# Optimization experiments

Measured on AMD Instinct MI355X. Metric: run time of the kernel, lower is better.

## Reference

```python
import jax, jax.numpy as jnp
import numpy as np
import math

DIM = 1024
NUM_HEADS = 16
HEAD_DIM = DIM // NUM_HEADS
BLOCK_SIZE = 64


def _block_mask(src_blocks, tgt_blocks, num_blocks):
    # Block-level BigBird mask: global first/last block columns, sliding window of 1, random blocks.
    i = jnp.arange(num_blocks)[:, None]
    j = jnp.arange(num_blocks)[None, :]
    band = jnp.abs(i - j) <= 1
    glob = (j == 0) | (j == num_blocks - 1)
    bm = band | glob
    bm = bm.at[src_blocks, tgt_blocks].set(True)
    return bm  # [nb, nb] bool


def setup_inputs() -> dict:
    key = jax.random.key(0)
    ks = jax.random.split(key, 12)
    B, S = 2, 2048
    x = jax.random.normal(ks[0], (B, S, DIM), dtype=jnp.float32)
    scale = 0.02
    Wq = jax.random.normal(ks[1], (DIM, DIM), dtype=jnp.float32) * scale
    bq = jnp.zeros((DIM,), dtype=jnp.float32)
    Wk = jax.random.normal(ks[2], (DIM, DIM), dtype=jnp.float32) * scale
    bk = jnp.zeros((DIM,), dtype=jnp.float32)
    Wv = jax.random.normal(ks[3], (DIM, DIM), dtype=jnp.float32) * scale
    bv = jnp.zeros((DIM,), dtype=jnp.float32)
    Wo = jax.random.normal(ks[4], (DIM, DIM), dtype=jnp.float32) * scale
    bo = jnp.zeros((DIM,), dtype=jnp.float32)
    num_blocks = S // BLOCK_SIZE
    src_blocks = jax.random.randint(ks[5], (3,), 0, num_blocks, dtype=jnp.int32)
    tgt_blocks = jax.random.randint(ks[6], (3,), 0, num_blocks, dtype=jnp.int32)
    return {"x": x, "Wq": Wq, "bq": bq, "Wk": Wk, "bk": bk, "Wv": Wv, "bv": bv,
            "Wo": Wo, "bo": bo, "src_blocks": src_blocks, "tgt_blocks": tgt_blocks}


def reference(x, Wq, bq, Wk, bk, Wv, bv, Wo, bo, src_blocks, tgt_blocks):
    B, S, _ = x.shape
    nb = S // BLOCK_SIZE
    # NOTE: original torch code uses .view (not transpose) to split heads; replicate faithfully.
    q = (x @ Wq.T + bq).reshape(B, NUM_HEADS, S, HEAD_DIM)
    k = (x @ Wk.T + bk).reshape(B, NUM_HEADS, S, HEAD_DIM)
    v = (x @ Wv.T + bv).reshape(B, NUM_HEADS, S, HEAD_DIM)
    bm = _block_mask(src_blocks, tgt_blocks, nb)
    mask = jnp.repeat(jnp.repeat(bm, BLOCK_SIZE, axis=0), BLOCK_SIZE, axis=1)  # [S, S]
    scores = jnp.einsum('bhqd,bhkd->bhqk', q, k) / math.sqrt(HEAD_DIM)
    scores = jnp.where(mask[None, None], scores, jnp.float32(-1e9))
    attn = jax.nn.softmax(scores, axis=-1)
    out = jnp.einsum('bhqk,bhkd->bhqd', attn, v)
    out = out.transpose(0, 2, 1, 3).reshape(B, S, DIM)
    return out @ Wo.T + bo
```

## Files before the change

kernel.cpp:

```cpp
#include <hip/hip_runtime.h>
#include <math.h>

typedef __attribute__((ext_vector_type(8))) short short8;
typedef __attribute__((ext_vector_type(4))) float f32x4;

#define SEQ 2048
#define NB  32

__device__ __forceinline__ unsigned short f2bf(float f) {
    unsigned u = __float_as_uint(f);
    u = (u + 0x7FFFu + ((u >> 16) & 1u)) >> 16;
    return (unsigned short)u;
}

__device__ __forceinline__ void gload16(const unsigned short* g, unsigned short* l) {
    __builtin_amdgcn_global_load_lds(
        (__attribute__((address_space(1))) void*)(void*)(g),
        (__attribute__((address_space(3))) void*)(l), 16, 0, 0);
}

__global__ __launch_bounds__(256) void cvt_bf16(const float* __restrict__ in,
                                                unsigned short* __restrict__ out, int n8) {
    int i = blockIdx.x * 256 + threadIdx.x;
    const int stride = gridDim.x * 256;
    for (; i < n8; i += stride) {
        const float4 a = ((const float4*)in)[i * 2];
        const float4 b = ((const float4*)in)[i * 2 + 1];
        uint4 o;
        o.x = f2bf(a.x) | ((unsigned)f2bf(a.y) << 16);
        o.y = f2bf(a.z) | ((unsigned)f2bf(a.w) << 16);
        o.z = f2bf(b.x) | ((unsigned)f2bf(b.y) << 16);
        o.w = f2bf(b.z) | ((unsigned)f2bf(b.w) << 16);
        ((uint4*)out)[i] = o;
    }
}

__global__ __launch_bounds__(256) void cvt_w4(const float* __restrict__ w0,
                                              const float* __restrict__ w1,
                                              const float* __restrict__ w2,
                                              const float* __restrict__ w3,
                                              unsigned short* __restrict__ o0,
                                              unsigned short* __restrict__ o1,
                                              unsigned short* __restrict__ o2,
                                              unsigned short* __restrict__ o3) {
    const int which = blockIdx.y;
    const float* in = (which == 0) ? w0 : (which == 1) ? w1 : (which == 2) ? w2 : w3;
    unsigned short* out = (which == 0) ? o0 : (which == 1) ? o1 : (which == 2) ? o2 : o3;
    int i = blockIdx.x * 256 + threadIdx.x;
    const int stride = gridDim.x * 256;
    for (; i < 131072; i += stride) {
        const float4 a = ((const float4*)in)[i * 2];
        const float4 b = ((const float4*)in)[i * 2 + 1];
        uint4 o;
        o.x = f2bf(a.x) | ((unsigned)f2bf(a.y) << 16);
        o.y = f2bf(a.z) | ((unsigned)f2bf(a.w) << 16);
        o.z = f2bf(b.x) | ((unsigned)f2bf(b.y) << 16);
        o.w = f2bf(b.z) | ((unsigned)f2bf(b.w) << 16);
        ((uint4*)out)[i] = o;
    }
}

template <int BF16OUT, int BN>
__global__ __launch_bounds__(256) void gemm_bt(const unsigned short* __restrict__ A,
                                               const unsigned short* __restrict__ Wall,
                                               const float* __restrict__ b0,
                                               const float* __restrict__ b1,
                                               const float* __restrict__ b2,
                                               unsigned short* __restrict__ outb,
                                               float* __restrict__ outf) {
    constexpr int MI = (BN == 128) ? 4 : 2;
    constexpr int NI = 4;
    __shared__ __align__(16) unsigned short As[2][128 * 32];
    __shared__ __align__(16) unsigned short Bs[2][BN * 32];

    const int t = threadIdx.x;
    const int w = t >> 6, l = t & 63;
    const int bx = blockIdx.x;
    const int which = (BN == 128) ? (bx >> 3) : 0;
    const int n0 = (BN == 128) ? (bx & 7) * 128 : bx * 64;
    const int m0 = blockIdx.y * 128;
    const unsigned short* W = Wall + (size_t)which * (1024ull * 1024);
    const float* bias = (which == 0) ? b0 : (which == 1) ? b1 : b2;

    const int wr = (BN == 128) ? (w >> 1) * 64 : w * 32;
    const int wc = (BN == 128) ? (w & 1) * 64 : 0;

    f32x4 acc[MI][NI];
#pragma unroll
    for (int i = 0; i < MI; ++i)
#pragma unroll
        for (int j = 0; j < NI; ++j) acc[i][j] = f32x4{0.f, 0.f, 0.f, 0.f};

    const unsigned short* Ag = A + (size_t)(m0 + w * 32 + (l >> 2)) * 1024 + (l & 3) * 8;
    const unsigned short* Wg =
        W + (size_t)(n0 + ((BN == 128) ? w * 32 : w * 16) + (l >> 2)) * 1024 + (l & 3) * 8;

    auto STAGE = [&](unsigned short* Asb, unsigned short* Bsb, int k0) {
        gload16(Ag + k0, Asb + w * 1024);
        gload16(Ag + k0 + 16 * 1024, Asb + w * 1024 + 512);
        gload16(Wg + k0, Bsb + ((BN == 128) ? w * 1024 : w * 512));
        if (BN == 128) gload16(Wg + k0 + 16 * 1024, Bsb + w * 1024 + 512);
    };
    auto COMPUTE = [&](const unsigned short* Asb, const unsigned short* Bsb) {
        short8 af[MI], bfr[NI];
#pragma unroll
        for (int mi = 0; mi < MI; ++mi)
            af[mi] = *(const short8*)&Asb[(wr + mi * 16 + (l & 15)) * 32 + (l >> 4) * 8];
#pragma unroll
        for (int ni = 0; ni < NI; ++ni)
            bfr[ni] = *(const short8*)&Bsb[(wc + ni * 16 + (l & 15)) * 32 + (l >> 4) * 8];
#pragma unroll
        for (int mi = 0; mi < MI; ++mi)
#pragma unroll
            for (int ni = 0; ni < NI; ++ni)
                acc[mi][ni] = __builtin_amdgcn_mfma_f32_16x16x32_bf16(af[mi], bfr[ni],
                                                                      acc[mi][ni], 0, 0, 0);
    };
#define WAITV_INFLIGHT()                                                  \
    do {                                                                  \
        if constexpr (BN == 128)                                          \
            asm volatile("s_waitcnt vmcnt(4)" ::: "memory");              \
        else                                                              \
            asm volatile("s_waitcnt vmcnt(3)" ::: "memory");              \
        __builtin_amdgcn_sched_barrier(0);                                \
    } while (0)
#define BAR()                                                             \
    do {                                                                  \
        __builtin_amdgcn_s_barrier();                                     \
        __builtin_amdgcn_sched_barrier(0);                                \
    } while (0)
#define READS_DONE_BAR()                                                  \
    do {                                                                  \
        asm volatile("s_waitcnt lgkmcnt(0)" ::: "memory");                \
        __builtin_amdgcn_sched_barrier(0);                                \
        __builtin_amdgcn_s_barrier();                                     \
        __builtin_amdgcn_sched_barrier(0);                                \
    } while (0)

    STAGE(As[0], Bs[0], 0);
#pragma unroll 1
    for (int kt2 = 0; kt2 < 16; ++kt2) {
        STAGE(As[1], Bs[1], (kt2 * 2 + 1) * 32);
        WAITV_INFLIGHT();
        BAR();
        COMPUTE(As[0], Bs[0]);
        READS_DONE_BAR();

        if (kt2 < 15) {
            STAGE(As[0], Bs[0], (kt2 * 2 + 2) * 32);
            WAITV_INFLIGHT();
        } else {
            asm volatile("s_waitcnt vmcnt(0)" ::: "memory");
            __builtin_amdgcn_sched_barrier(0);
        }
        BAR();
        COMPUTE(As[1], Bs[1]);
        if (kt2 < 15) READS_DONE_BAR();
    }
#undef WAITV_INFLIGHT
#undef BAR
#undef READS_DONE_BAR

    const int g = l >> 4, c = l & 15;
#pragma unroll
    for (int ni = 0; ni < NI; ++ni) {
        const int n = n0 + wc + ni * 16 + c;
        const float bv = bias[n];
#pragma unroll
        for (int mi = 0; mi < MI; ++mi) {
#pragma unroll
            for (int j = 0; j < 4; ++j) {
                const size_t m = (size_t)(m0 + wr + mi * 16 + g * 4 + j);
                const float v = acc[mi][ni][j] + bv;
                if (BF16OUT)
                    (outb + (size_t)which * (4096ull * 1024))[m * 1024 + n] = f2bf(v);
                else
                    outf[m * 1024 + n] = v;
            }
        }
    }
}

__global__ __launch_bounds__(256) void transpose_v(const unsigned short* __restrict__ v,
                                                   unsigned short* __restrict__ vt) {
    __shared__ __align__(16) unsigned short L[64][72];
    const int t = threadIdx.x;
    const int st = blockIdx.x;
    const int ht = blockIdx.y;
    const int b = blockIdx.z;
    {
        const int r = t >> 2, cs = t & 3;
        const unsigned short* src =
            v + (size_t)(b * 16 + ht) * (SEQ * 64) + (size_t)(st * 64 + r) * 64 + cs * 16;
        *(uint4*)&L[r][cs * 16] = *(const uint4*)src;
        *(uint4*)&L[r][cs * 16 + 8] = *(const uint4*)(src + 8);
    }
    __syncthreads();
    {
        const int dr = t >> 2, ss = t & 3;
        unsigned short tmp[16];
#pragma unroll
        for (int e = 0; e < 16; ++e) tmp[e] = L[ss * 16 + e][dr];
        unsigned short* dst =
            vt + (size_t)(b * 16 + ht) * (SEQ * 64) + (size_t)dr * SEQ + st * 64 + ss * 16;
        *(uint4*)dst = *(uint4*)&tmp[0];
        *(uint4*)(dst + 8) = *(uint4*)&tmp[8];
    }
}

__global__ __launch_bounds__(256) void attn_mfma(const unsigned short* __restrict__ qb_,
                                                 const unsigned short* __restrict__ kb_,
                                                 const unsigned short* __restrict__ vtb_,
                                                 const int* __restrict__ srcb,
                                                 const int* __restrict__ tgtb,
                                                 unsigned short* __restrict__ outb) {
    __shared__ __align__(16) unsigned short Ks[64 * 72];
    __shared__ __align__(16) unsigned short Vs[64 * 72];
    __shared__ __align__(16) unsigned short Ps[4][16 * 72];

    const int t = threadIdx.x, w = t >> 6, l = t & 63;
    const int qi = blockIdx.x, h = blockIdx.y, b = blockIdx.z;
    const int g = l >> 4, c = l & 15;

    unsigned mask = 1u | (1u << (NB - 1)) | (1u << qi);
    if (qi > 0) mask |= 1u << (qi - 1);
    if (qi < NB - 1) mask |= 1u << (qi + 1);
#pragma unroll
    for (int tt = 0; tt < 3; ++tt)
        if (srcb[tt] == qi) mask |= 1u << (tgtb[tt] & 31);

    const size_t ho = (size_t)(b * 16 + h) * (SEQ * 64);
    const unsigned short* Q = qb_ + ho;
    const unsigned short* K = kb_ + ho;
    const unsigned short* VT = vtb_ + ho;

    short8 qf[2];
    {
        const unsigned short* qrow = Q + (size_t)(qi * 64 + w * 16 + c) * 64;
        qf[0] = *(const short8*)(qrow + g * 8);
        qf[1] = *(const short8*)(qrow + 32 + g * 8);
    }

    f32x4 oacc[4];
#pragma unroll
    for (int d = 0; d < 4; ++d) oacc[d] = f32x4{0.f, 0.f, 0.f, 0.f};
    float mrun = -INFINITY, lsum = 0.f;

    const int sr = t >> 2, sc = (t & 3) * 16;

    for (int kb = 0; kb < NB; ++kb) {
        if (!((mask >> kb) & 1u)) continue;

        const unsigned short* ksrc = K + (size_t)(kb * 64 + sr) * 64 + sc;
        const unsigned short* vsrc = VT + (size_t)sr * SEQ + kb * 64 + sc;
        uint4 k0 = *(const uint4*)ksrc, k1 = *(const uint4*)(ksrc + 8);
        uint4 v0 = *(const uint4*)vsrc, v1 = *(const uint4*)(vsrc + 8);

        __syncthreads();
        *(uint4*)&Ks[sr * 72 + sc] = k0;
        *(uint4*)&Ks[sr * 72 + sc + 8] = k1;
        *(uint4*)&Vs[sr * 72 + sc] = v0;
        *(uint4*)&Vs[sr * 72 + sc + 8] = v1;
        __syncthreads();

        f32x4 sacc[4];
#pragma unroll
        for (int kt = 0; kt < 4; ++kt) sacc[kt] = f32x4{0.f, 0.f, 0.f, 0.f};
#pragma unroll
        for (int kt = 0; kt < 4; ++kt) {
#pragma unroll
            for (int ks = 0; ks < 2; ++ks) {
                const short8 ka = *(const short8*)&Ks[(kt * 16 + c) * 72 + ks * 32 + g * 8];
                sacc[kt] = __builtin_amdgcn_mfma_f32_16x16x32_bf16(ka, qf[ks], sacc[kt], 0, 0, 0);
            }
        }

        float sv[16];
        float tmax = -INFINITY;
#pragma unroll
        for (int kt = 0; kt < 4; ++kt)
#pragma unroll
            for (int j = 0; j < 4; ++j) {
                const float x = sacc[kt][j] * 0.125f;
                sv[kt * 4 + j] = x;
                tmax = fmaxf(tmax, x);
            }
        tmax = fmaxf(tmax, __shfl_xor(tmax, 16));
        tmax = fmaxf(tmax, __shfl_xor(tmax, 32));
        const float newm = fmaxf(mrun, tmax);
        const float corr = __expf(mrun - newm);
        float ps = 0.f;
#pragma unroll
        for (int e = 0; e < 16; ++e) {
            const float p = __expf(sv[e] - newm);
            sv[e] = p;
            ps += p;
        }
        ps += __shfl_xor(ps, 16);
        ps += __shfl_xor(ps, 32);
        lsum = lsum * corr + ps;
        mrun = newm;
#pragma unroll
        for (int d = 0; d < 4; ++d)
#pragma unroll
            for (int j = 0; j < 4; ++j) oacc[d][j] *= corr;

        unsigned short* pw = &Ps[w][c * 72];
#pragma unroll
        for (int kt = 0; kt < 4; ++kt) {
            uint2 pk;
            pk.x = f2bf(sv[kt * 4 + 0]) | ((unsigned)f2bf(sv[kt * 4 + 1]) << 16);
            pk.y = f2bf(sv[kt * 4 + 2]) | ((unsigned)f2bf(sv[kt * 4 + 3]) << 16);
            *(uint2*)&pw[kt * 16 + g * 4] = pk;
        }
        asm volatile("s_waitcnt lgkmcnt(0)" ::: "memory");
        __builtin_amdgcn_sched_barrier(0);

#pragma unroll
        for (int ks = 0; ks < 2; ++ks) {
            const short8 pb = *(const short8*)&Ps[w][c * 72 + ks * 32 + g * 8];
#pragma unroll
            for (int dt = 0; dt < 4; ++dt) {
                const short8 va = *(const short8*)&Vs[(dt * 16 + c) * 72 + ks * 32 + g * 8];
                oacc[dt] = __builtin_amdgcn_mfma_f32_16x16x32_bf16(va, pb, oacc[dt], 0, 0, 0);
            }
        }
    }

    const float inv = 1.f / lsum;
    unsigned short* orow = outb + (size_t)(b * SEQ + qi * 64 + w * 16 + c) * 1024 + h * 64;
#pragma unroll
    for (int dt = 0; dt < 4; ++dt)
#pragma unroll
        for (int j = 0; j < 4; ++j)
            orow[dt * 16 + g * 4 + j] = f2bf(oacc[dt][j] * inv);
}

extern "C" void kernel_launch(void* const* d_in, const int* in_sizes, int n_in,
                              void* d_out, int out_size, void* d_ws, size_t ws_size,
                              hipStream_t stream) {
    const float* x  = (const float*)d_in[0];
    const float* Wq = (const float*)d_in[1];
    const float* bq = (const float*)d_in[2];
    const float* Wk = (const float*)d_in[3];
    const float* bk = (const float*)d_in[4];
    const float* Wv = (const float*)d_in[5];
    const float* bv = (const float*)d_in[6];
    const float* Wo = (const float*)d_in[7];
    const float* bo = (const float*)d_in[8];
    const int* srcb = (const int*)d_in[9];
    const int* tgtb = (const int*)d_in[10];

    unsigned short* wsu = (unsigned short*)d_ws;
    unsigned short* xbf   = wsu;
    unsigned short* wqkv  = wsu + 4194304ull;
    unsigned short* wobf  = wsu + 7340032ull;
    unsigned short* qkvbf = wsu + 8388608ull;
    unsigned short* vtbf  = wsu + 20971520ull;
    unsigned short* attbf = wsu + 25165824ull;

    hipLaunchKernelGGL(cvt_bf16, dim3(1024), dim3(256), 0, stream, x, xbf, 524288);
    hipLaunchKernelGGL(cvt_w4, dim3(512, 4), dim3(256), 0, stream,
                       Wq, Wk, Wv, Wo,
                       wqkv, wqkv + 1048576ull, wqkv + 2097152ull, wobf);

    hipLaunchKernelGGL((gemm_bt<1, 128>), dim3(24, 32), dim3(256), 0, stream,
                       xbf, wqkv, bq, bk, bv, qkvbf, (float*)nullptr);

    hipLaunchKernelGGL(transpose_v, dim3(32, 16, 2), dim3(256), 0, stream,
                       qkvbf + 2ull * 4194304ull, vtbf);

    hipLaunchKernelGGL(attn_mfma, dim3(32, 16, 2), dim3(256), 0, stream,
                       qkvbf, qkvbf + 4194304ull, vtbf, srcb, tgtb, attbf);

    hipLaunchKernelGGL((gemm_bt<0, 64>), dim3(16, 32), dim3(256), 0, stream,
                       attbf, wobf, bo, bo, bo, (unsigned short*)nullptr, (float*)d_out);

    (void)in_sizes; (void)n_in; (void)out_size; (void)ws_size;
}
```

Measured before the change: 97.06 us.

## Fuse V transpose into attention LDS staging and merge conversion kernels

Drops the standalone V transpose kernel. The attention kernel now reads V in its natural row layout and transposes it while storing into shared memory, using scalar 16-bit LDS writes. The x and weight bf16 conversions are also merged into one launch with a 5-row grid. This removes a kernel launch and a full round trip of V through global memory, at the cost of many narrow, possibly bank-conflicting LDS stores in the attention inner loop.

```diff
diff --git a/kernel.cpp b/kernel.cpp
--- a/kernel.cpp
+++ b/kernel.cpp
@@ -19,36 +19,25 @@
         (__attribute__((address_space(3))) void*)(l), 16, 0, 0);
 }
 
-__global__ __launch_bounds__(256) void cvt_bf16(const float* __restrict__ in,
-                                                unsigned short* __restrict__ out, int n8) {
+__global__ __launch_bounds__(256) void cvt_all(const float* __restrict__ x,
+                                               const float* __restrict__ w0,
+                                               const float* __restrict__ w1,
+                                               const float* __restrict__ w2,
+                                               const float* __restrict__ w3,
+                                               unsigned short* __restrict__ ox,
+                                               unsigned short* __restrict__ o0,
+                                               unsigned short* __restrict__ o1,
+                                               unsigned short* __restrict__ o2,
+                                               unsigned short* __restrict__ o3) {
+    const int which = blockIdx.y;
+    const float* in = (which == 0) ? x : (which == 1) ? w0 : (which == 2) ? w1
+                       : (which == 3) ? w2 : w3;
+    unsigned short* out = (which == 0) ? ox : (which == 1) ? o0 : (which == 2) ? o1
+                          : (which == 3) ? o2 : o3;
+    const int n8 = (which == 0) ? 524288 : 131072;
     int i = blockIdx.x * 256 + threadIdx.x;
     const int stride = gridDim.x * 256;
     for (; i < n8; i += stride) {
-        const float4 a = ((const float4*)in)[i * 2];
-        const float4 b = ((const float4*)in)[i * 2 + 1];
-        uint4 o;
-        o.x = f2bf(a.x) | ((unsigned)f2bf(a.y) << 16);
-        o.y = f2bf(a.z) | ((unsigned)f2bf(a.w) << 16);
-        o.z = f2bf(b.x) | ((unsigned)f2bf(b.y) << 16);
-        o.w = f2bf(b.z) | ((unsigned)f2bf(b.w) << 16);
-        ((uint4*)out)[i] = o;
-    }
-}
-
-__global__ __launch_bounds__(256) void cvt_w4(const float* __restrict__ w0,
-                                              const float* __restrict__ w1,
-                                              const float* __restrict__ w2,
-                                              const float* __restrict__ w3,
-                                              unsigned short* __restrict__ o0,
-                                              unsigned short* __restrict__ o1,
-                                              unsigned short* __restrict__ o2,
-                                              unsigned short* __restrict__ o3) {
-    const int which = blockIdx.y;
-    const float* in = (which == 0) ? w0 : (which == 1) ? w1 : (which == 2) ? w2 : w3;
-    unsigned short* out = (which == 0) ? o0 : (which == 1) ? o1 : (which == 2) ? o2 : o3;
-    int i = blockIdx.x * 256 + threadIdx.x;
-    const int stride = gridDim.x * 256;
-    for (; i < 131072; i += stride) {
         const float4 a = ((const float4*)in)[i * 2];
         const float4 b = ((const float4*)in)[i * 2 + 1];
         uint4 o;
@@ -181,36 +170,9 @@
     }
 }
 
-__global__ __launch_bounds__(256) void transpose_v(const unsigned short* __restrict__ v,
-                                                   unsigned short* __restrict__ vt) {
-    __shared__ __align__(16) unsigned short L[64][72];
-    const int t = threadIdx.x;
-    const int st = blockIdx.x;
-    const int ht = blockIdx.y;
-    const int b = blockIdx.z;
-    {
-        const int r = t >> 2, cs = t & 3;
-        const unsigned short* src =
-            v + (size_t)(b * 16 + ht) * (SEQ * 64) + (size_t)(st * 64 + r) * 64 + cs * 16;
-        *(uint4*)&L[r][cs * 16] = *(const uint4*)src;
-        *(uint4*)&L[r][cs * 16 + 8] = *(const uint4*)(src + 8);
-    }
-    __syncthreads();
-    {
-        const int dr = t >> 2, ss = t & 3;
-        unsigned short tmp[16];
-#pragma unroll
-        for (int e = 0; e < 16; ++e) tmp[e] = L[ss * 16 + e][dr];
-        unsigned short* dst =
-            vt + (size_t)(b * 16 + ht) * (SEQ * 64) + (size_t)dr * SEQ + st * 64 + ss * 16;
-        *(uint4*)dst = *(uint4*)&tmp[0];
-        *(uint4*)(dst + 8) = *(uint4*)&tmp[8];
-    }
-}
-
 __global__ __launch_bounds__(256) void attn_mfma(const unsigned short* __restrict__ qb_,
                                                  const unsigned short* __restrict__ kb_,
-                                                 const unsigned short* __restrict__ vtb_,
+                                                 const unsigned short* __restrict__ vb_,
                                                  const int* __restrict__ srcb,
                                                  const int* __restrict__ tgtb,
                                                  unsigned short* __restrict__ outb) {
@@ -232,7 +194,7 @@
     const size_t ho = (size_t)(b * 16 + h) * (SEQ * 64);
     const unsigned short* Q = qb_ + ho;
     const unsigned short* K = kb_ + ho;
-    const unsigned short* VT = vtb_ + ho;
+    const unsigned short* V = vb_ + ho;
 
     short8 qf[2];
     {
@@ -252,15 +214,22 @@
         if (!((mask >> kb) & 1u)) continue;
 
         const unsigned short* ksrc = K + (size_t)(kb * 64 + sr) * 64 + sc;
-        const unsigned short* vsrc = VT + (size_t)sr * SEQ + kb * 64 + sc;
+        const unsigned short* vsrc = V + (size_t)(kb * 64 + sr) * 64 + sc;
         uint4 k0 = *(const uint4*)ksrc, k1 = *(const uint4*)(ksrc + 8);
         uint4 v0 = *(const uint4*)vsrc, v1 = *(const uint4*)(vsrc + 8);
 
         __syncthreads();
         *(uint4*)&Ks[sr * 72 + sc] = k0;
         *(uint4*)&Ks[sr * 72 + sc + 8] = k1;
-        *(uint4*)&Vs[sr * 72 + sc] = v0;
-        *(uint4*)&Vs[sr * 72 + sc + 8] = v1;
+        {
+            const unsigned short* p0 = (const unsigned short*)&v0;
+            const unsigned short* p1 = (const unsigned short*)&v1;
+#pragma unroll
+            for (int e = 0; e < 8; ++e) {
+                Vs[(sc + e) * 72 + sr] = p0[e];
+                Vs[(sc + 8 + e) * 72 + sr] = p1[e];
+            }
+        }
         __syncthreads();
 
         f32x4 sacc[4];
@@ -356,22 +325,18 @@
     unsigned short* wqkv  = wsu + 4194304ull;
     unsigned short* wobf  = wsu + 7340032ull;
     unsigned short* qkvbf = wsu + 8388608ull;
-    unsigned short* vtbf  = wsu + 20971520ull;
     unsigned short* attbf = wsu + 25165824ull;
 
-    hipLaunchKernelGGL(cvt_bf16, dim3(1024), dim3(256), 0, stream, x, xbf, 524288);
-    hipLaunchKernelGGL(cvt_w4, dim3(512, 4), dim3(256), 0, stream,
-                       Wq, Wk, Wv, Wo,
-                       wqkv, wqkv + 1048576ull, wqkv + 2097152ull, wobf);
+    hipLaunchKernelGGL(cvt_all, dim3(512, 5), dim3(256), 0, stream,
+                       x, Wq, Wk, Wv, Wo,
+                       xbf, wqkv, wqkv + 1048576ull, wqkv + 2097152ull, wobf);
 
     hipLaunchKernelGGL((gemm_bt<1, 128>), dim3(24, 32), dim3(256), 0, stream,
                        xbf, wqkv, bq, bk, bv, qkvbf, (float*)nullptr);
 
-    hipLaunchKernelGGL(transpose_v, dim3(32, 16, 2), dim3(256), 0, stream,
-                       qkvbf + 2ull * 4194304ull, vtbf);
-
     hipLaunchKernelGGL(attn_mfma, dim3(32, 16, 2), dim3(256), 0, stream,
-                       qkvbf, qkvbf + 4194304ull, vtbf, srcb, tgtb, attbf);
+                       qkvbf, qkvbf + 4194304ull, qkvbf + 2ull * 4194304ull,
+                       srcb, tgtb, attbf);
 
     hipLaunchKernelGGL((gemm_bt<0, 64>), dim3(16, 32), dim3(256), 0, stream,
                        attbf, wobf, bo, bo, bo, (unsigned short*)nullptr, (float*)d_out);
```

Measured after the change: 92.82 us. -4.4%, faster.
